# Kernel optimization log

Hardware: AMD Instinct MI355X
Metric: run time of the kernel (lower is better)

The kernel has to match this reference:

```python
import jax, jax.numpy as jnp
import numpy as np

THR = 0.2
POOL_A = 160
POOL_B = 96
EPS = 1e-5


def _adaptive_avg_pool_last(x, out_size):
    # torch AdaptiveAvgPool1d semantics: bin i averages [floor(i*n/o), ceil((i+1)*n/o))
    n = x.shape[-1]
    i = np.arange(out_size)
    starts = (i * n) // out_size
    ends = -((-(i + 1) * n) // out_size)
    cs = jnp.cumsum(x, axis=-1)
    cs = jnp.concatenate([jnp.zeros_like(cs[..., :1]), cs], axis=-1)
    sums = cs[..., ends] - cs[..., starts]
    return sums / jnp.asarray(ends - starts, x.dtype)


def _unfold3x3(x, H, W):
    # Faithful to torch: raw reshape (N, L, C) -> (N, C, H, W) (memory reinterpretation,
    # NOT a transpose), then F.unfold(k=3, pad=1) and rearrange 'n (c ww) l -> n l ww c'.
    N, L, C = x.shape
    img = x.reshape(N, C, H, W)
    pad = jnp.pad(img, ((0, 0), (0, 0), (1, 1), (1, 1)))
    # window positions in row-major (ky, kx) order, matching F.unfold
    patches = jnp.stack([pad[:, :, dy:dy + H, dx:dx + W]
                         for dy in range(3) for dx in range(3)], axis=2)  # (N,C,9,H,W)
    return patches.transpose(0, 3, 4, 2, 1).reshape(N, H * W, 9, C)  # (N,L,9,C)


def _forward(feat_s0, feat_s1, ln_weight, ln_bias):
    N, L, C = feat_s0.shape
    H = W = int(round(L ** 0.5))
    conf = jnp.einsum('nlc,nsc->nls', feat_s0, feat_s1) / (C ** 0.5)
    conf = jax.nn.softmax(conf, axis=1) * jax.nn.softmax(conf, axis=2)
    # mutual nearest-neighbor mask with confidence threshold
    mask = ((conf > THR)
            & (conf == conf.max(axis=2, keepdims=True))
            & (conf == conf.max(axis=1, keepdims=True))).astype(feat_s0.dtype)
    u0 = _unfold3x3(feat_s0, H, W)
    u1 = _unfold3x3(feat_s1, H, W)
    sem0 = jnp.einsum('nlc,nlwc->nlw', feat_s0, u0) / C  # divided by C (shape[-1]), as in source
    sem1 = jnp.einsum('nlc,nlwc->nlw', feat_s1, u1) / C
    fea0 = jnp.einsum('nlwc,nlw->nlc', u0, sem0)
    fea1 = jnp.einsum('nlwc,nlw->nlc', u1, sem1)
    s0 = jnp.einsum('nls,nsd->nld', mask, fea1) / L
    s1 = jnp.einsum('nsl,nsd->nld', mask, fea0) / L
    f0 = jnp.concatenate([_adaptive_avg_pool_last(feat_s0, POOL_A),
                          _adaptive_avg_pool_last(s0, POOL_B)], axis=-1)
    f1 = jnp.concatenate([_adaptive_avg_pool_last(feat_s1, POOL_A),
                          _adaptive_avg_pool_last(s1, POOL_B)], axis=-1)
    f = jnp.concatenate([f0, f1], axis=0)  # (2N, L, 256)
    mu = f.mean(-1, keepdims=True)
    var = f.var(-1, keepdims=True)
    f = (f - mu) * jax.lax.rsqrt(var + EPS) * ln_weight + ln_bias
    return f[:N], f[N:]


def setup_inputs():
    key = jax.random.key(0)
    k0, k1 = jax.random.split(key)
    N, L, C = 2, 4096, 256
    return {
        'feat_s0': jax.random.normal(k0, (N, L, C), jnp.float32),
        'feat_s1': jax.random.normal(k1, (N, L, C), jnp.float32),
        'ln_weight': jnp.ones((C,), jnp.float32),
        'ln_bias': jnp.zeros((C,), jnp.float32),
    }


def reference(feat_s0, feat_s1, ln_weight, ln_bias):
    return _forward(feat_s0, feat_s1, ln_weight, ln_bias)
```

## Files before the change

### kernel.cpp

```cpp
#include <hip/hip_runtime.h>
#include <stdint.h>

#define NBATCH 2
#define LL 4096
#define CC 256
#define LSTR8 144
#define KEXP 0.09016844f
#define KEXP2 0.18033688f
#define IMIN (-2147483647 - 1)

typedef long i64f;
typedef float f32x4 __attribute__((ext_vector_type(4)));

#if defined(__has_builtin) && __has_builtin(__builtin_amdgcn_exp2f)
#define EXP2F(x) __builtin_amdgcn_exp2f(x)
#else
#define EXP2F(x) exp2f(x)
#endif

__global__ __launch_bounds__(256) void cast_fp8(
    const float* __restrict__ a, const float* __restrict__ b,
    uint32_t* __restrict__ oa, uint32_t* __restrict__ ob){
  int idx = blockIdx.x * 256 + threadIdx.x;
  float4 va = ((const float4*)a)[idx];
  float4 vb = ((const float4*)b)[idx];
  int ra = __builtin_amdgcn_cvt_pk_fp8_f32(va.x, va.y, 0, false);
  ra = __builtin_amdgcn_cvt_pk_fp8_f32(va.z, va.w, ra, true);
  int rb = __builtin_amdgcn_cvt_pk_fp8_f32(vb.x, vb.y, 0, false);
  rb = __builtin_amdgcn_cvt_pk_fp8_f32(vb.z, vb.w, rb, true);
  oa[idx] = (uint32_t)ra;
  ob[idx] = (uint32_t)rb;
}

__global__ __launch_bounds__(256) void conf_pass(
    const uint8_t* __restrict__ f0q, const uint8_t* __restrict__ f1q,
    float* __restrict__ rowSum, float* __restrict__ colSum,
    int* __restrict__ rowPart, int* __restrict__ colPart){
  __shared__ uint8_t Alds[128*LSTR8], Blds[128*LSTR8];
  float* rowS = (float*)Alds;
  float* colS = (float*)(Alds + 1024);
  int*   rb   = (int*)  (Alds + 2048);
  int*   cb   = (int*)  (Alds + 3072);
  int st = blockIdx.x, lt = blockIdx.y, n = blockIdx.z;
  int t = threadIdx.x;
  const int wv = t >> 6, lane = t & 63, lr = lane & 15, quad = lane >> 4;
  const int lq = wv >> 1, sq = wv & 1;
  const uint8_t* A = f0q + (size_t)n*LL*CC;
  const uint8_t* B = f1q + (size_t)n*LL*CC;
  f32x4 acc[4][4];
  #pragma unroll
  for (int r = 0; r < 4; r++)
    #pragma unroll
    for (int j = 0; j < 4; j++) acc[r][j] = (f32x4){0.f,0.f,0.f,0.f};
  for (int kc = 0; kc < 2; kc++){
    __syncthreads();
    #pragma unroll
    for (int m = 0; m < 8; m++){
      int f = m*256 + t, row = f >> 4, kg = f & 15;
      *(uint2*)(Alds + row*LSTR8 + kg*8) =
          *(const uint2*)(A + (size_t)(lt*128 + row)*CC + kc*128 + kg*8);
      *(uint2*)(Blds + row*LSTR8 + kg*8) =
          *(const uint2*)(B + (size_t)(st*128 + row)*CC + kc*128 + kg*8);
    }
    __syncthreads();
    #pragma unroll
    for (int kk = 0; kk < 4; kk++){
      i64f a[4], b[4];
      #pragma unroll
      for (int r = 0; r < 4; r++)
        a[r] = *(const i64f*)(Alds + (lq*64 + r*16 + lr)*LSTR8 + kk*32 + quad*8);
      #pragma unroll
      for (int j = 0; j < 4; j++)
        b[j] = *(const i64f*)(Blds + (sq*64 + j*16 + lr)*LSTR8 + kk*32 + quad*8);
      #pragma unroll
      for (int r = 0; r < 4; r++)
        #pragma unroll
        for (int j = 0; j < 4; j++)
          acc[r][j] = __builtin_amdgcn_mfma_f32_16x16x32_fp8_fp8(a[r], b[j], acc[r][j], 0, 0, 0);
    }
  }
  const int sbase = st*128 + sq*64 + lr;
  const int lbase = lt*128 + lq*64 + quad*4;
  float rsum[4][4], csum[4] = {0.f,0.f,0.f,0.f};
  int rkey[4][4], ckey[4] = {IMIN,IMIN,IMIN,IMIN};
  #pragma unroll
  for (int r = 0; r < 4; r++)
    #pragma unroll
    for (int rr = 0; rr < 4; rr++){ rsum[r][rr] = 0.f; rkey[r][rr] = IMIN; }
  #pragma unroll
  for (int r = 0; r < 4; r++)
    #pragma unroll
    for (int j = 0; j < 4; j++)
      #pragma unroll
      for (int rr = 0; rr < 4; rr++){
        float a = acc[r][j][rr];
        float e = EXP2F(a * KEXP);
        rsum[r][rr] += e;
        csum[j] += e;
        int iqs = ((int)(a * 2048.f)) << 12;
        rkey[r][rr] = max(rkey[r][rr], iqs + (sbase + j*16));
        ckey[j]     = max(ckey[j],     iqs + (lbase + r*16 + rr));
      }
  #pragma unroll
  for (int msk = 1; msk <= 8; msk <<= 1)
    #pragma unroll
    for (int r = 0; r < 4; r++)
      #pragma unroll
      for (int rr = 0; rr < 4; rr++){
        rsum[r][rr] += __shfl_xor(rsum[r][rr], msk);
        rkey[r][rr] = max(rkey[r][rr], __shfl_xor(rkey[r][rr], msk));
      }
  #pragma unroll
  for (int msk = 16; msk <= 32; msk <<= 1)
    #pragma unroll
    for (int j = 0; j < 4; j++){
      csum[j] += __shfl_xor(csum[j], msk);
      ckey[j] = max(ckey[j], __shfl_xor(ckey[j], msk));
    }
  __syncthreads();
  if (lr == 0){
    #pragma unroll
    for (int r = 0; r < 4; r++)
      #pragma unroll
      for (int rr = 0; rr < 4; rr++){
        int row = lq*64 + r*16 + quad*4 + rr;
        rowS[sq*128 + row] = rsum[r][rr];
        rb[sq*128 + row]   = rkey[r][rr];
      }
  }
  if (quad == 0){
    #pragma unroll
    for (int j = 0; j < 4; j++){
      int col = sq*64 + j*16 + lr;
      colS[lq*128 + col] = csum[j];
      cb[lq*128 + col]   = ckey[j];
    }
  }
  __syncthreads();
  if (t < 128){
    rowSum[((size_t)n*LL + lt*128 + t)*32 + st] = rowS[t] + rowS[128 + t];
    colSum[((size_t)n*LL + st*128 + t)*32 + lt] = colS[t] + colS[128 + t];
    rowPart[((size_t)n*LL + lt*128 + t)*32 + st] = max(rb[t], rb[128 + t]);
    colPart[((size_t)n*LL + st*128 + t)*32 + lt] = max(cb[t], cb[128 + t]);
  }
}

__device__ float fea_fly(const float* __restrict__ featn, int srow, int t){
  __shared__ float sred[9][4];
  __shared__ float ssem[9];
  int lane = t & 63, wv = t >> 6;
  int h = srow >> 6, xx = srow & 63;
  float fv = featn[(size_t)srow * CC + t];
  float uv[9];
  #pragma unroll
  for (int w = 0; w < 9; w++){
    int dy = w/3 - 1, dx = w%3 - 1;
    int y = h + dy, x = xx + dx;
    uv[w] = (y >= 0 && y < 64 && x >= 0 && x < 64) ? featn[(size_t)t * 4096 + y*64 + x] : 0.f;
  }
  __syncthreads();
  #pragma unroll
  for (int w = 0; w < 9; w++){
    float pvv = fv * uv[w];
    #pragma unroll
    for (int msk = 1; msk <= 32; msk <<= 1) pvv += __shfl_xor(pvv, msk);
    if (lane == 0) sred[w][wv] = pvv;
  }
  __syncthreads();
  if (t < 9) ssem[t] = (sred[t][0] + sred[t][1] + sred[t][2] + sred[t][3]) * (1.f/256.f);
  __syncthreads();
  float acc = 0.f;
  #pragma unroll
  for (int w = 0; w < 9; w++) acc += uv[w] * ssem[w];
  __syncthreads();
  return acc;
}

__device__ __forceinline__ float pool_window(const float* f, const float* s, int t){
  if (t < 160){
    int a = (t*8)/5, e = (t*8+12)/5;
    float sum = 0.f;
    for (int i = a; i < e; i++) sum += f[i];
    return sum / (float)(e - a);
  } else {
    int tt = t - 160;
    int a = (tt*8)/3, e = (tt*8+10)/3;
    float sum = 0.f;
    for (int i = a; i < e; i++) sum += s[i];
    return sum / (float)(e - a);
  }
}

__global__ __launch_bounds__(256) void tail(
    const float* __restrict__ feat0, const float* __restrict__ feat1,
    const float* __restrict__ rowSum, const float* __restrict__ colSum,
    const int* __restrict__ rowPart, const int* __restrict__ colPart,
    const float* __restrict__ lnw, const float* __restrict__ lnb,
    float* __restrict__ out){
  int l = blockIdx.x, n = blockIdx.y, t = threadIdx.x;
  int lane = t & 63, wv = t >> 6;
  size_t base = (size_t)n * LL;
  __shared__ float sVal[8];
  {
    float s = 0.f; int k = IMIN;
    if (lane < 32){
      size_t off = (base + l)*32 + lane;
      if      (wv == 0) s = rowSum[off];
      else if (wv == 1) s = colSum[off];
      else if (wv == 2) k = rowPart[off];
      else              k = colPart[off];
    }
    #pragma unroll
    for (int msk = 1; msk <= 16; msk <<= 1){
      s += __shfl_xor(s, msk);
      k = max(k, __shfl_xor(k, msk));
    }
    if (lane == 0) sVal[wv] = (wv < 2) ? s : __int_as_float(k);
  }
  __syncthreads();
  int rowK = __float_as_int(sVal[2]), colK = __float_as_int(sVal[3]);
  int ssr = rowK & 4095, ssc = colK & 4095;
  {
    float s = 0.f; int k = IMIN;
    if (lane < 32){
      if      (wv == 0) s = colSum [(base + ssr)*32 + lane];
      else if (wv == 1) s = rowSum [(base + ssc)*32 + lane];
      else if (wv == 2) k = colPart[(base + ssr)*32 + lane];
      else              k = rowPart[(base + ssc)*32 + lane];
    }
    #pragma unroll
    for (int msk = 1; msk <= 16; msk <<= 1){
      s += __shfl_xor(s, msk);
      k = max(k, __shfl_xor(k, msk));
    }
    if (lane == 0) sVal[4 + wv] = (wv < 2) ? s : __int_as_float(k);
  }
  __syncthreads();
  float Rl   = sVal[0], Cl   = sVal[1];
  float Cssr = sVal[4], Rssc = sVal[5];
  int ck2 = __float_as_int(sVal[6]), rk2 = __float_as_int(sVal[7]);
  float v0 = 0.f, v1 = 0.f;
  {
    float araw = (float)(rowK >> 12) * (1.f/2048.f);
    float val = exp2f(araw * KEXP2) / (Rl * Cssr);
    if (val > 0.2f && (ck2 & 4095) == l)
      v0 = fea_fly(feat1 + (size_t)n*LL*CC, ssr, t) * (1.f/4096.f);
  }
  {
    float araw = (float)(colK >> 12) * (1.f/2048.f);
    float val = exp2f(araw * KEXP2) / (Cl * Rssc);
    if (val > 0.2f && (rk2 & 4095) == l)
      v1 = fea_fly(feat0 + (size_t)n*LL*CC, ssc, t) * (1.f/4096.f);
  }
  __shared__ float f0r[CC], f1r[CC], s0r[CC], s1r[CC];
  __shared__ float redA[2][4], redB[2][4];
  f0r[t] = feat0[(base + l)*CC + t];
  f1r[t] = feat1[(base + l)*CC + t];
  s0r[t] = v0;
  s1r[t] = v1;
  __syncthreads();
  float pA = pool_window(f0r, s0r, t);
  float pB = pool_window(f1r, s1r, t);
  float smA = pA, sqA = pA*pA, smB = pB, sqB = pB*pB;
  #pragma unroll
  for (int msk = 1; msk <= 32; msk <<= 1){
    smA += __shfl_xor(smA, msk);
    sqA += __shfl_xor(sqA, msk);
    smB += __shfl_xor(smB, msk);
    sqB += __shfl_xor(sqB, msk);
  }
  if (lane == 0){ redA[0][wv] = smA; redA[1][wv] = sqA; redB[0][wv] = smB; redB[1][wv] = sqB; }
  __syncthreads();
  float tsA = redA[0][0]+redA[0][1]+redA[0][2]+redA[0][3];
  float tqA = redA[1][0]+redA[1][1]+redA[1][2]+redA[1][3];
  float tsB = redB[0][0]+redB[0][1]+redB[0][2]+redB[0][3];
  float tqB = redB[1][0]+redB[1][1]+redB[1][2]+redB[1][3];
  float muA = tsA * (1.f/256.f), varA = tqA * (1.f/256.f) - muA*muA;
  float muB = tsB * (1.f/256.f), varB = tqB * (1.f/256.f) - muB*muB;
  float w = lnw[t], bsh = lnb[t];
  out[((size_t)n*LL + l)*CC + t]       = (pA - muA) * rsqrtf(varA + 1e-5f) * w + bsh;
  out[((size_t)(2 + n)*LL + l)*CC + t] = (pB - muB) * rsqrtf(varB + 1e-5f) * w + bsh;
}

extern "C" void kernel_launch(void* const* d_in, const int* in_sizes, int n_in,
                              void* d_out, int out_size, void* d_ws, size_t ws_size,
                              hipStream_t stream){
  const float* feat0 = (const float*)d_in[0];
  const float* feat1 = (const float*)d_in[1];
  const float* lnw   = (const float*)d_in[2];
  const float* lnb   = (const float*)d_in[3];
  float* out = (float*)d_out;
  char* ws = (char*)d_ws;
  const size_t MB = 1024 * 1024;
  uint8_t* f0q = (uint8_t*)(ws + 0);
  uint8_t* f1q = (uint8_t*)(ws + 2*MB);
  float* rowSum  = (float*)(ws + 4*MB);
  float* colSum  = (float*)(ws + 5*MB);
  int*   rowPart = (int*)  (ws + 6*MB);
  int*   colPart = (int*)  (ws + 7*MB);

  cast_fp8<<<2048, 256, 0, stream>>>(feat0, feat1, (uint32_t*)f0q, (uint32_t*)f1q);
  dim3 gconf(32, 32, NBATCH);
  conf_pass<<<gconf, 256, 0, stream>>>(f0q, f1q, rowSum, colSum, rowPart, colPart);
  dim3 gt(LL, NBATCH);
  tail<<<gt, 256, 0, stream>>>(feat0, feat1, rowSum, colSum, rowPart, colPart,
                               lnw, lnb, out);
}
```

Measured before the change: 136.0 us.

## Prefetch second K-chunk into registers, swizzle block order, hoist tail loads

In conf_pass, the second K-chunk (columns 128..255) of both fp8 operand tiles is loaded into registers while the first chunk is being multiplied, then written to LDS. This overlaps global-load latency with MFMA work. The linear block index is also remapped across interleaved groups to change L2 locality, and launch bounds now request 4 blocks per CU. In the tail kernel, the feature-row and layer-norm parameter loads are moved to the start so their latency hides behind the reductions. The register prefetch raises register pressure, which may conflict with the occupancy hint.

```diff
diff --git a/kernel.cpp b/kernel.cpp
--- a/kernel.cpp
+++ b/kernel.cpp
@@ -32,7 +32,7 @@
   ob[idx] = (uint32_t)rb;
 }
 
-__global__ __launch_bounds__(256) void conf_pass(
+__global__ __launch_bounds__(256, 4) void conf_pass(
     const uint8_t* __restrict__ f0q, const uint8_t* __restrict__ f1q,
     float* __restrict__ rowSum, float* __restrict__ colSum,
     int* __restrict__ rowPart, int* __restrict__ colPart){
@@ -41,44 +41,63 @@
   float* colS = (float*)(Alds + 1024);
   int*   rb   = (int*)  (Alds + 2048);
   int*   cb   = (int*)  (Alds + 3072);
-  int st = blockIdx.x, lt = blockIdx.y, n = blockIdx.z;
+  int bl = (blockIdx.z*32 + blockIdx.y)*32 + blockIdx.x;
+  int nb = (bl & 7)*256 + (bl >> 3);
+  int st = nb & 31, lt = (nb >> 5) & 31, n = nb >> 10;
   int t = threadIdx.x;
   const int wv = t >> 6, lane = t & 63, lr = lane & 15, quad = lane >> 4;
   const int lq = wv >> 1, sq = wv & 1;
-  const uint8_t* A = f0q + (size_t)n*LL*CC;
-  const uint8_t* B = f1q + (size_t)n*LL*CC;
+  const uint8_t* A = f0q + (size_t)n*LL*CC + (size_t)(lt*128)*CC;
+  const uint8_t* B = f1q + (size_t)n*LL*CC + (size_t)(st*128)*CC;
   f32x4 acc[4][4];
   #pragma unroll
   for (int r = 0; r < 4; r++)
     #pragma unroll
     for (int j = 0; j < 4; j++) acc[r][j] = (f32x4){0.f,0.f,0.f,0.f};
-  for (int kc = 0; kc < 2; kc++){
-    __syncthreads();
-    #pragma unroll
-    for (int m = 0; m < 8; m++){
-      int f = m*256 + t, row = f >> 4, kg = f & 15;
-      *(uint2*)(Alds + row*LSTR8 + kg*8) =
-          *(const uint2*)(A + (size_t)(lt*128 + row)*CC + kc*128 + kg*8);
-      *(uint2*)(Blds + row*LSTR8 + kg*8) =
-          *(const uint2*)(B + (size_t)(st*128 + row)*CC + kc*128 + kg*8);
-    }
-    __syncthreads();
+
+  auto compute = [&](){
     #pragma unroll
     for (int kk = 0; kk < 4; kk++){
-      i64f a[4], b[4];
+      i64f a[4], bf[4];
       #pragma unroll
       for (int r = 0; r < 4; r++)
         a[r] = *(const i64f*)(Alds + (lq*64 + r*16 + lr)*LSTR8 + kk*32 + quad*8);
       #pragma unroll
       for (int j = 0; j < 4; j++)
-        b[j] = *(const i64f*)(Blds + (sq*64 + j*16 + lr)*LSTR8 + kk*32 + quad*8);
+        bf[j] = *(const i64f*)(Blds + (sq*64 + j*16 + lr)*LSTR8 + kk*32 + quad*8);
       #pragma unroll
       for (int r = 0; r < 4; r++)
         #pragma unroll
         for (int j = 0; j < 4; j++)
-          acc[r][j] = __builtin_amdgcn_mfma_f32_16x16x32_fp8_fp8(a[r], b[j], acc[r][j], 0, 0, 0);
-    }
-  }
+          acc[r][j] = __builtin_amdgcn_mfma_f32_16x16x32_fp8_fp8(a[r], bf[j], acc[r][j], 0, 0, 0);
+    }
+  };
+
+  #pragma unroll
+  for (int m = 0; m < 8; m++){
+    int f = m*256 + t, row = f >> 4, kg = f & 15;
+    *(uint2*)(Alds + row*LSTR8 + kg*8) = *(const uint2*)(A + (size_t)row*CC + kg*8);
+    *(uint2*)(Blds + row*LSTR8 + kg*8) = *(const uint2*)(B + (size_t)row*CC + kg*8);
+  }
+  uint2 pa[8], pb[8];
+  #pragma unroll
+  for (int m = 0; m < 8; m++){
+    int f = m*256 + t, row = f >> 4, kg = f & 15;
+    pa[m] = *(const uint2*)(A + (size_t)row*CC + 128 + kg*8);
+    pb[m] = *(const uint2*)(B + (size_t)row*CC + 128 + kg*8);
+  }
+  __syncthreads();
+  compute();
+  __syncthreads();
+  #pragma unroll
+  for (int m = 0; m < 8; m++){
+    int f = m*256 + t, row = f >> 4, kg = f & 15;
+    *(uint2*)(Alds + row*LSTR8 + kg*8) = pa[m];
+    *(uint2*)(Blds + row*LSTR8 + kg*8) = pb[m];
+  }
+  __syncthreads();
+  compute();
+
   const int sbase = st*128 + sq*64 + lr;
   const int lbase = lt*128 + lq*64 + quad*4;
   float rsum[4][4], csum[4] = {0.f,0.f,0.f,0.f};
@@ -200,6 +219,9 @@
   int l = blockIdx.x, n = blockIdx.y, t = threadIdx.x;
   int lane = t & 63, wv = t >> 6;
   size_t base = (size_t)n * LL;
+  float fv0 = feat0[(base + l)*CC + t];
+  float fv1 = feat1[(base + l)*CC + t];
+  float w = lnw[t], bsh = lnb[t];
   __shared__ float sVal[8];
   {
     float s = 0.f; int k = IMIN;
@@ -254,8 +276,8 @@
   }
   __shared__ float f0r[CC], f1r[CC], s0r[CC], s1r[CC];
   __shared__ float redA[2][4], redB[2][4];
-  f0r[t] = feat0[(base + l)*CC + t];
-  f1r[t] = feat1[(base + l)*CC + t];
+  f0r[t] = fv0;
+  f1r[t] = fv1;
   s0r[t] = v0;
   s1r[t] = v1;
   __syncthreads();
@@ -277,7 +299,6 @@
   float tqB = redB[1][0]+redB[1][1]+redB[1][2]+redB[1][3];
   float muA = tsA * (1.f/256.f), varA = tqA * (1.f/256.f) - muA*muA;
   float muB = tsB * (1.f/256.f), varB = tqB * (1.f/256.f) - muB*muB;
-  float w = lnw[t], bsh = lnb[t];
   out[((size_t)n*LL + l)*CC + t]       = (pA - muA) * rsqrtf(varA + 1e-5f) * w + bsh;
   out[((size_t)(2 + n)*LL + l)*CC + t] = (pB - muB) * rsqrtf(varB + 1e-5f) * w + bsh;
 }
```

Result: no change. 137.7 us (+1.2%).
